# Kernel optimization log

Hardware: AMD Instinct MI355X
Metric: run time of the kernel (lower is better)

## Reference

```python
import jax, jax.numpy as jnp
import numpy as np

N, F, E, B, D = 100000, 256, 128, 10000, 32
GAMMA, ZETA = -0.1, 1.1  # hard-concrete stretch params of L0Dense


def setup_inputs() -> dict:
    key = jax.random.key(0)
    ks = jax.random.split(key, 12)
    return {
        "nodes": jax.random.randint(ks[0], (B,), 0, N),
        "neigh_idx": jax.random.randint(ks[1], (B, D), 0, N),
        "neigh_mask": jax.random.bernoulli(ks[2], 0.9, (B, D)),
        "feature": jax.random.normal(ks[3], (N, F), jnp.float32),
        "W": jax.random.normal(ks[4], (F, E), jnp.float32) * 0.05,
        "b": jnp.zeros((E,), jnp.float32),
        "qz_loga": jax.random.normal(ks[5], (F,), jnp.float32),
        "att1_w": jax.random.normal(ks[6], (2 * E, E), jnp.float32) * 0.05,
        "att1_b": jnp.zeros((E,), jnp.float32),
        "att2_w": jax.random.normal(ks[7], (E, E), jnp.float32) * 0.05,
        "att2_b": jnp.zeros((E,), jnp.float32),
        "att3_w": jax.random.normal(ks[8], (E, 1), jnp.float32) * 0.05,
        "att3_b": jnp.zeros((1,), jnp.float32),
    }


def reference(nodes, neigh_idx, neigh_mask, feature, W, b, qz_loga,
              att1_w, att1_b, att2_w, att2_b, att3_w, att3_b):
    # L0Dense, deterministic (eval) hard-concrete gate on input dims
    z = jnp.clip(jax.nn.sigmoid(qz_loga) * (ZETA - GAMMA) + GAMMA, 0.0, 1.0)
    We = W * z[:, None]                                  # [F, E]

    node_feat = feature[nodes] @ We + b                   # [B, E]
    neigh_feat = feature[neigh_idx] @ We + b              # [B, D, E]

    # GraphRec-style attention MLP over (neighbor, center) pairs
    h = jnp.concatenate(
        [neigh_feat, jnp.broadcast_to(node_feat[:, None, :], neigh_feat.shape)],
        axis=-1)                                          # [B, D, 2E]
    h = jax.nn.relu(h @ att1_w + att1_b)
    h = jax.nn.relu(h @ att2_w + att2_b)
    scores = (h @ att3_w + att3_b)[..., 0]                # [B, D]
    scores = jnp.where(neigh_mask, scores, -1e30)
    att = jax.nn.softmax(scores, axis=-1)                 # [B, D]

    agg = jnp.einsum('bd,bde->be', att, neigh_feat)       # weighted sum
    has_neigh = neigh_mask.any(axis=-1, keepdims=True)
    return jnp.where(has_neigh, agg, node_feat)           # n==0 fallback
```

## Files before the change

### kernel.cpp

```cpp
#include <hip/hip_runtime.h>
#include <hip/hip_bf16.h>
#include <math.h>

#define NN 100000
#define FF 256
#define EE 128
#define BB_ 10000
#define DD 32

typedef __attribute__((ext_vector_type(8))) short short8;
typedef __attribute__((ext_vector_type(4))) float f32x4;

__device__ __forceinline__ short f2bf(float f) {
  union { float f; unsigned u; } v; v.f = f;
  unsigned r = v.u + 0x7fffu + ((v.u >> 16) & 1u);
  return (short)(r >> 16);
}
__device__ __forceinline__ float bf2f(short s) {
  union { unsigned u; float f; } v;
  v.u = ((unsigned)(unsigned short)s) << 16;
  return v.f;
}

__global__ __launch_bounds__(256) void k_prep(
    const float* __restrict__ W, const float* __restrict__ qz,
    const float* __restrict__ a1w, const float* __restrict__ a2w,
    short* __restrict__ WeT, short* __restrict__ a1wTn,
    short* __restrict__ a1wTc, short* __restrict__ w2T) {
  int i = blockIdx.x * 256 + threadIdx.x;
  if (i < 32768) {
    int e = i >> 8, f = i & 255;
    float g = qz[f];
    float s = 1.0f / (1.0f + expf(-g));
    float z = fminf(fmaxf(s * 1.2f - 0.1f, 0.0f), 1.0f);
    WeT[e * 256 + f] = f2bf(W[f * 128 + e] * z);
  } else if (i < 49152) {
    int t = i - 32768; int n = t >> 7, k = t & 127;
    a1wTn[n * 128 + k] = f2bf(a1w[k * 128 + n]);
  } else if (i < 65536) {
    int t = i - 49152; int n = t >> 7, k = t & 127;
    a1wTc[n * 128 + k] = f2bf(a1w[(128 + k) * 128 + n]);
  } else if (i < 81920) {
    int t = i - 65536; int n = t >> 7, k = t & 127;
    w2T[n * 128 + k] = f2bf(a2w[k * 128 + n]);
  }
}

template <int K, bool AF32, bool OUTBF16>
__global__ __launch_bounds__(256) void k_mm(
    const void* __restrict__ Ap, const short* __restrict__ BT,
    const float* __restrict__ bias, const int* __restrict__ idx,
    void* __restrict__ Cp, int M) {
  __shared__ short As[128 * 64];
  __shared__ short Bs[128 * 64];
  const int tid = threadIdx.x;
  const int mb = blockIdx.x * 128;
  const int wave = tid >> 6, lane = tid & 63;
  const int wr = wave >> 1, wc = wave & 1;
  const int l15 = lane & 15, lg = lane >> 4;

  size_t abase[4];
#pragma unroll
  for (int s = 0; s < 4; ++s) {
    int row = (tid + s * 256) >> 3;
    int grow = mb + row;
    int gr = 0;
    if (grow < M) gr = idx ? idx[grow] : grow;
    abase[s] = (size_t)gr * K;
  }

  f32x4 acc[4][4];
#pragma unroll
  for (int i = 0; i < 4; ++i)
#pragma unroll
    for (int j = 0; j < 4; ++j) acc[i][j] = (f32x4){0.f, 0.f, 0.f, 0.f};

  for (int k0 = 0; k0 < K; k0 += 64) {
#pragma unroll
    for (int s = 0; s < 4; ++s) {
      int q = tid + s * 256;
      int row = q >> 3, c = q & 7;
      short8 av;
      if (AF32) {
        const float* ap = (const float*)Ap + abase[s] + k0 + c * 8;
        float4 f0 = *(const float4*)ap;
        float4 f1 = *(const float4*)(ap + 4);
        av[0] = f2bf(f0.x); av[1] = f2bf(f0.y);
        av[2] = f2bf(f0.z); av[3] = f2bf(f0.w);
        av[4] = f2bf(f1.x); av[5] = f2bf(f1.y);
        av[6] = f2bf(f1.z); av[7] = f2bf(f1.w);
      } else {
        av = *(const short8*)((const short*)Ap + abase[s] + k0 + c * 8);
      }
      *(short8*)(As + row * 64 + 8 * (c ^ (row & 7))) = av;
      short8 bv = *(const short8*)(BT + (size_t)row * K + k0 + c * 8);
      *(short8*)(Bs + row * 64 + 8 * (c ^ (row & 7))) = bv;
    }
    __syncthreads();
#pragma unroll
    for (int ks = 0; ks < 2; ++ks) {
      int c = ks * 4 + lg;
      short8 af[4], bfv[4];
#pragma unroll
      for (int i = 0; i < 4; ++i) {
        int r = wr * 64 + i * 16 + l15;
        af[i] = *(short8*)(As + r * 64 + 8 * (c ^ (r & 7)));
        int n = wc * 64 + i * 16 + l15;
        bfv[i] = *(short8*)(Bs + n * 64 + 8 * (c ^ (n & 7)));
      }
#pragma unroll
      for (int i = 0; i < 4; ++i)
#pragma unroll
        for (int j = 0; j < 4; ++j)
          acc[i][j] = __builtin_amdgcn_mfma_f32_16x16x32_bf16(
              af[i], bfv[j], acc[i][j], 0, 0, 0);
    }
    __syncthreads();
  }

  float bv4[4];
#pragma unroll
  for (int j = 0; j < 4; ++j) {
    int col = wc * 64 + j * 16 + l15;
    bv4[j] = bias ? bias[col] : 0.f;
  }
#pragma unroll
  for (int i = 0; i < 4; ++i) {
#pragma unroll
    for (int r = 0; r < 4; ++r) {
      int row = mb + wr * 64 + i * 16 + lg * 4 + r;
      if (row < M) {
#pragma unroll
        for (int j = 0; j < 4; ++j) {
          int col = wc * 64 + j * 16 + l15;
          float v = acc[i][j][r] + bv4[j];
          if (OUTBF16)
            ((short*)Cp)[(size_t)row * EE + col] = f2bf(v);
          else
            ((float*)Cp)[(size_t)row * EE + col] = v;
        }
      }
    }
  }
}

__global__ __launch_bounds__(256) void k_attn2(
    const short* __restrict__ X, const short* __restrict__ Y,
    const float* __restrict__ P, const int* __restrict__ nodes,
    const int* __restrict__ nidx, const int* __restrict__ nmask,
    const short* __restrict__ w2T, const float* __restrict__ b2,
    const float* __restrict__ w3, const float* __restrict__ b3,
    float* __restrict__ out) {
  __shared__ short h1s[128 * 128];
  __shared__ int nidx_s[128];
  __shared__ float scores_s[256];
  __shared__ float atts_s[128];
  __shared__ int has_sh[4];
  const int tid = threadIdx.x;
  const int b0 = blockIdx.x * 4;
  const int wave = tid >> 6, lane = tid & 63;
  const int wr = wave >> 1, wc = wave & 1;
  const int l15 = lane & 15, lg = lane >> 4;

  if (tid < 128) nidx_s[tid] = nidx[b0 * DD + tid];
  __syncthreads();

#pragma unroll
  for (int s = 0; s < 8; ++s) {
    int q = tid + s * 256;
    int row = q >> 4, c = q & 15;
    int n = nidx_s[row];
    short8 yv = *(const short8*)(Y + (size_t)n * EE + c * 8);
    const float* pp = P + (size_t)(b0 + (row >> 5)) * EE + c * 8;
    float4 p0 = *(const float4*)pp;
    float4 p1 = *(const float4*)(pp + 4);
    float pf[8] = {p0.x, p0.y, p0.z, p0.w, p1.x, p1.y, p1.z, p1.w};
    short8 hv;
#pragma unroll
    for (int j = 0; j < 8; ++j)
      hv[j] = f2bf(fmaxf(bf2f(yv[j]) + pf[j], 0.f));
    *(short8*)(h1s + row * 128 + 8 * ((c & 8) | ((c ^ row) & 7))) = hv;
  }
  __syncthreads();

  f32x4 acc[4][4];
#pragma unroll
  for (int i = 0; i < 4; ++i)
#pragma unroll
    for (int j = 0; j < 4; ++j) acc[i][j] = (f32x4){0.f, 0.f, 0.f, 0.f};

#pragma unroll
  for (int ks = 0; ks < 4; ++ks) {
    int c = ks * 4 + lg;
    short8 af[4], bfv[4];
#pragma unroll
    for (int i = 0; i < 4; ++i) {
      int r = wr * 64 + i * 16 + l15;
      af[i] = *(short8*)(h1s + r * 128 + 8 * ((c & 8) | ((c ^ r) & 7)));
      int n = wc * 64 + i * 16 + l15;
      bfv[i] = *(const short8*)(w2T + n * 128 + c * 8);
    }
#pragma unroll
    for (int i = 0; i < 4; ++i)
#pragma unroll
      for (int j = 0; j < 4; ++j)
        acc[i][j] = __builtin_amdgcn_mfma_f32_16x16x32_bf16(
            af[i], bfv[j], acc[i][j], 0, 0, 0);
  }

  float b2v[4], w3v[4];
#pragma unroll
  for (int j = 0; j < 4; ++j) {
    int col = wc * 64 + j * 16 + l15;
    b2v[j] = b2[col];
    w3v[j] = w3[col];
  }
  float part[16];
#pragma unroll
  for (int i = 0; i < 4; ++i)
#pragma unroll
    for (int r = 0; r < 4; ++r) {
      float s = 0.f;
#pragma unroll
      for (int j = 0; j < 4; ++j)
        s += fmaxf(acc[i][j][r] + b2v[j], 0.f) * w3v[j];
      part[i * 4 + r] = s;
    }
#pragma unroll
  for (int off = 1; off <= 8; off <<= 1) {
#pragma unroll
    for (int t = 0; t < 16; ++t) part[t] += __shfl_xor(part[t], off);
  }
  if (l15 == 0) {
#pragma unroll
    for (int i = 0; i < 4; ++i)
#pragma unroll
      for (int r = 0; r < 4; ++r) {
        int row = wr * 64 + i * 16 + lg * 4 + r;
        scores_s[row * 2 + wc] = part[i * 4 + r];
      }
  }
  __syncthreads();

  float b3v = b3[0];
  if (lane < 32) {
    int row = wave * 32 + lane;
    int m = nmask[(size_t)(b0 + wave) * DD + lane];
    float s = scores_s[row * 2] + scores_s[row * 2 + 1] + b3v;
    if (!m) s = -1e30f;
    float mx = s;
#pragma unroll
    for (int off = 1; off <= 16; off <<= 1) mx = fmaxf(mx, __shfl_xor(mx, off));
    float e = expf(s - mx);
    float sum = e;
#pragma unroll
    for (int off = 1; off <= 16; off <<= 1) sum += __shfl_xor(sum, off);
    atts_s[row] = e / sum;
    unsigned long long bal = __ballot(m != 0);
    if (lane == 0) has_sh[wave] = (bal != 0ull) ? 1 : 0;
  }
  __syncthreads();

  {
    int g = wave;
    float a0 = 0.f, a1 = 0.f;
    if (has_sh[g]) {
#pragma unroll 4
      for (int d = 0; d < 32; ++d) {
        float a = atts_s[g * 32 + d];
        const short* xr = X + (size_t)nidx_s[g * 32 + d] * EE;
        a0 += a * bf2f(xr[lane]);
        a1 += a * bf2f(xr[lane + 64]);
      }
    } else {
      const short* xr = X + (size_t)nodes[b0 + g] * EE;
      a0 = bf2f(xr[lane]);
      a1 = bf2f(xr[lane + 64]);
    }
    out[(size_t)(b0 + g) * EE + lane] = a0;
    out[(size_t)(b0 + g) * EE + lane + 64] = a1;
  }
}

extern "C" void kernel_launch(void* const* d_in, const int* in_sizes, int n_in,
                              void* d_out, int out_size, void* d_ws,
                              size_t ws_size, hipStream_t stream) {
  const int* nodes = (const int*)d_in[0];
  const int* nidx = (const int*)d_in[1];
  const int* nmask = (const int*)d_in[2];
  const float* feature = (const float*)d_in[3];
  const float* W = (const float*)d_in[4];
  const float* bb = (const float*)d_in[5];
  const float* qz = (const float*)d_in[6];
  const float* a1w = (const float*)d_in[7];
  const float* a1b = (const float*)d_in[8];
  const float* a2w = (const float*)d_in[9];
  const float* a2b = (const float*)d_in[10];
  const float* a3w = (const float*)d_in[11];
  const float* a3b = (const float*)d_in[12];
  float* out = (float*)d_out;

  char* ws = (char*)d_ws;
  short* WeT   = (short*)(ws);
  short* a1wTn = (short*)(ws + 65536);
  short* a1wTc = (short*)(ws + 98304);
  short* w2T   = (short*)(ws + 131072);
  short* Xb    = (short*)(ws + 163840);
  short* Yb    = (short*)(ws + 163840 + 25600000);
  float* Pv    = (float*)(ws + 163840 + 51200000);

  k_prep<<<320, 256, 0, stream>>>(W, qz, a1w, a2w, WeT, a1wTn, a1wTc, w2T);
  k_mm<256, true, true><<<(NN + 127) / 128, 256, 0, stream>>>(
      feature, WeT, bb, nullptr, Xb, NN);
  k_mm<128, false, true><<<(NN + 127) / 128, 256, 0, stream>>>(
      Xb, a1wTn, a1b, nullptr, Yb, NN);
  k_mm<128, false, false><<<(BB_ + 127) / 128, 256, 0, stream>>>(
      Xb, a1wTc, nullptr, nodes, Pv, BB_);
  k_attn2<<<BB_ / 4, 256, 0, stream>>>(Xb, Yb, Pv, nodes, nidx, nmask, w2T,
                                       a2b, a3w, a3b, out);
}
```

Baseline: 123.8 us.

## Restructure attention kernel to one batch row per wave without LDS staging

The attention kernel now gives each wave one center node with its 32 neighbours. The first-layer activations are built directly in registers as MFMA A operands, instead of being staged through a 32KB swizzled LDS tile. This removes most shared memory use and all block-wide barriers. In exchange, each wave loads the full w2T B operand on its own. It relies on wave-synchronous LDS ordering for its small index and score arrays. The float-to-bf16 helper now uses the HIP intrinsic, and the gather and output stores are widened to 32-bit and float2 accesses.

Result: slower. 130.4 us (+5.3%).

```diff
diff --git a/kernel.cpp b/kernel.cpp
--- a/kernel.cpp
+++ b/kernel.cpp
@@ -12,9 +12,9 @@
 typedef __attribute__((ext_vector_type(4))) float f32x4;
 
 __device__ __forceinline__ short f2bf(float f) {
-  union { float f; unsigned u; } v; v.f = f;
-  unsigned r = v.u + 0x7fffu + ((v.u >> 16) & 1u);
-  return (short)(r >> 16);
+  __hip_bfloat16 h = __float2bfloat16(f);
+  union { __hip_bfloat16 h; short s; } u; u.h = h;
+  return u.s;
 }
 __device__ __forceinline__ float bf2f(short s) {
   union { unsigned u; float f; } v;
@@ -144,142 +144,128 @@
   }
 }
 
-__global__ __launch_bounds__(256) void k_attn2(
+__global__ __launch_bounds__(256) void k_attn3(
     const short* __restrict__ X, const short* __restrict__ Y,
     const float* __restrict__ P, const int* __restrict__ nodes,
     const int* __restrict__ nidx, const int* __restrict__ nmask,
     const short* __restrict__ w2T, const float* __restrict__ b2,
     const float* __restrict__ w3, const float* __restrict__ b3,
     float* __restrict__ out) {
-  __shared__ short h1s[128 * 128];
-  __shared__ int nidx_s[128];
-  __shared__ float scores_s[256];
-  __shared__ float atts_s[128];
-  __shared__ int has_sh[4];
+  __shared__ int ni_s[4][32];
+  __shared__ float sc_s[4][32];
+  __shared__ float att_s[4][32];
   const int tid = threadIdx.x;
-  const int b0 = blockIdx.x * 4;
   const int wave = tid >> 6, lane = tid & 63;
-  const int wr = wave >> 1, wc = wave & 1;
+  const int b = blockIdx.x * 4 + wave;
   const int l15 = lane & 15, lg = lane >> 4;
 
-  if (tid < 128) nidx_s[tid] = nidx[b0 * DD + tid];
-  __syncthreads();
-
-#pragma unroll
-  for (int s = 0; s < 8; ++s) {
-    int q = tid + s * 256;
-    int row = q >> 4, c = q & 15;
-    int n = nidx_s[row];
-    short8 yv = *(const short8*)(Y + (size_t)n * EE + c * 8);
-    const float* pp = P + (size_t)(b0 + (row >> 5)) * EE + c * 8;
-    float4 p0 = *(const float4*)pp;
-    float4 p1 = *(const float4*)(pp + 4);
-    float pf[8] = {p0.x, p0.y, p0.z, p0.w, p1.x, p1.y, p1.z, p1.w};
-    short8 hv;
+  if (lane < 32) ni_s[wave][lane] = nidx[b * DD + lane];
+
+  const int nid0 = ni_s[wave][l15];
+  const int nid1 = ni_s[wave][16 + l15];
+  const short* yr0 = Y + (size_t)nid0 * EE;
+  const short* yr1 = Y + (size_t)nid1 * EE;
+  const float* pr = P + (size_t)b * EE;
+
+  f32x4 acc[2][8];
+#pragma unroll
+  for (int i = 0; i < 2; ++i)
+#pragma unroll
+    for (int j = 0; j < 8; ++j) acc[i][j] = (f32x4){0.f, 0.f, 0.f, 0.f};
+
+#pragma unroll
+  for (int ks = 0; ks < 4; ++ks) {
+    const int k0 = ks * 32 + lg * 8;
+    short8 y0 = *(const short8*)(yr0 + k0);
+    short8 y1 = *(const short8*)(yr1 + k0);
+    float4 pa = *(const float4*)(pr + k0);
+    float4 pb = *(const float4*)(pr + k0 + 4);
+    float pf[8] = {pa.x, pa.y, pa.z, pa.w, pb.x, pb.y, pb.z, pb.w};
+    short8 a0, a1;
+#pragma unroll
+    for (int e = 0; e < 8; ++e) {
+      a0[e] = f2bf(fmaxf(bf2f(y0[e]) + pf[e], 0.f));
+      a1[e] = f2bf(fmaxf(bf2f(y1[e]) + pf[e], 0.f));
+    }
+    short8 bfv[8];
 #pragma unroll
     for (int j = 0; j < 8; ++j)
-      hv[j] = f2bf(fmaxf(bf2f(yv[j]) + pf[j], 0.f));
-    *(short8*)(h1s + row * 128 + 8 * ((c & 8) | ((c ^ row) & 7))) = hv;
-  }
-  __syncthreads();
-
-  f32x4 acc[4][4];
-#pragma unroll
-  for (int i = 0; i < 4; ++i)
-#pragma unroll
-    for (int j = 0; j < 4; ++j) acc[i][j] = (f32x4){0.f, 0.f, 0.f, 0.f};
-
-#pragma unroll
-  for (int ks = 0; ks < 4; ++ks) {
-    int c = ks * 4 + lg;
-    short8 af[4], bfv[4];
-#pragma unroll
-    for (int i = 0; i < 4; ++i) {
-      int r = wr * 64 + i * 16 + l15;
-      af[i] = *(short8*)(h1s + r * 128 + 8 * ((c & 8) | ((c ^ r) & 7)));
-      int n = wc * 64 + i * 16 + l15;
-      bfv[i] = *(const short8*)(w2T + n * 128 + c * 8);
-    }
-#pragma unroll
-    for (int i = 0; i < 4; ++i)
-#pragma unroll
-      for (int j = 0; j < 4; ++j)
-        acc[i][j] = __builtin_amdgcn_mfma_f32_16x16x32_bf16(
-            af[i], bfv[j], acc[i][j], 0, 0, 0);
-  }
-
-  float b2v[4], w3v[4];
-#pragma unroll
-  for (int j = 0; j < 4; ++j) {
-    int col = wc * 64 + j * 16 + l15;
+      bfv[j] = *(const short8*)(w2T + (size_t)(j * 16 + l15) * EE + k0);
+    __builtin_amdgcn_s_setprio(1);
+#pragma unroll
+    for (int j = 0; j < 8; ++j) {
+      acc[0][j] = __builtin_amdgcn_mfma_f32_16x16x32_bf16(a0, bfv[j],
+                                                          acc[0][j], 0, 0, 0);
+      acc[1][j] = __builtin_amdgcn_mfma_f32_16x16x32_bf16(a1, bfv[j],
+                                                          acc[1][j], 0, 0, 0);
+    }
+    __builtin_amdgcn_s_setprio(0);
+  }
+
+  float b2v[8], w3v[8];
+#pragma unroll
+  for (int j = 0; j < 8; ++j) {
+    int col = j * 16 + l15;
     b2v[j] = b2[col];
     w3v[j] = w3[col];
   }
-  float part[16];
-#pragma unroll
-  for (int i = 0; i < 4; ++i)
+  float part[2][4];
+#pragma unroll
+  for (int i = 0; i < 2; ++i)
 #pragma unroll
     for (int r = 0; r < 4; ++r) {
       float s = 0.f;
 #pragma unroll
-      for (int j = 0; j < 4; ++j)
+      for (int j = 0; j < 8; ++j)
         s += fmaxf(acc[i][j][r] + b2v[j], 0.f) * w3v[j];
-      part[i * 4 + r] = s;
+      part[i][r] = s;
     }
 #pragma unroll
   for (int off = 1; off <= 8; off <<= 1) {
 #pragma unroll
-    for (int t = 0; t < 16; ++t) part[t] += __shfl_xor(part[t], off);
+    for (int i = 0; i < 2; ++i)
+#pragma unroll
+      for (int r = 0; r < 4; ++r) part[i][r] += __shfl_xor(part[i][r], off);
   }
   if (l15 == 0) {
 #pragma unroll
-    for (int i = 0; i < 4; ++i)
-#pragma unroll
-      for (int r = 0; r < 4; ++r) {
-        int row = wr * 64 + i * 16 + lg * 4 + r;
-        scores_s[row * 2 + wc] = part[i * 4 + r];
-      }
-  }
-  __syncthreads();
-
-  float b3v = b3[0];
-  if (lane < 32) {
-    int row = wave * 32 + lane;
-    int m = nmask[(size_t)(b0 + wave) * DD + lane];
-    float s = scores_s[row * 2] + scores_s[row * 2 + 1] + b3v;
-    if (!m) s = -1e30f;
-    float mx = s;
-#pragma unroll
-    for (int off = 1; off <= 16; off <<= 1) mx = fmaxf(mx, __shfl_xor(mx, off));
-    float e = expf(s - mx);
-    float sum = e;
-#pragma unroll
-    for (int off = 1; off <= 16; off <<= 1) sum += __shfl_xor(sum, off);
-    atts_s[row] = e / sum;
-    unsigned long long bal = __ballot(m != 0);
-    if (lane == 0) has_sh[wave] = (bal != 0ull) ? 1 : 0;
-  }
-  __syncthreads();
-
-  {
-    int g = wave;
-    float a0 = 0.f, a1 = 0.f;
-    if (has_sh[g]) {
+    for (int i = 0; i < 2; ++i)
+#pragma unroll
+      for (int r = 0; r < 4; ++r)
+        sc_s[wave][i * 16 + lg * 4 + r] = part[i][r];
+  }
+
+  const int row = lane & 31;
+  const int m = nmask[(size_t)b * DD + row];
+  float s = sc_s[wave][row] + b3[0];
+  if (!m) s = -1e30f;
+  float mx = s;
+#pragma unroll
+  for (int off = 1; off <= 16; off <<= 1) mx = fmaxf(mx, __shfl_xor(mx, off));
+  float e = expf(s - mx);
+  float sum = e;
+#pragma unroll
+  for (int off = 1; off <= 16; off <<= 1) sum += __shfl_xor(sum, off);
+  if (lane < 32) att_s[wave][row] = e / sum;
+  const bool has = (__ballot(m != 0) != 0ull);
+
+  float a0 = 0.f, a1 = 0.f;
+  if (has) {
 #pragma unroll 4
-      for (int d = 0; d < 32; ++d) {
-        float a = atts_s[g * 32 + d];
-        const short* xr = X + (size_t)nidx_s[g * 32 + d] * EE;
-        a0 += a * bf2f(xr[lane]);
-        a1 += a * bf2f(xr[lane + 64]);
-      }
-    } else {
-      const short* xr = X + (size_t)nodes[b0 + g] * EE;
-      a0 = bf2f(xr[lane]);
-      a1 = bf2f(xr[lane + 64]);
-    }
-    out[(size_t)(b0 + g) * EE + lane] = a0;
-    out[(size_t)(b0 + g) * EE + lane + 64] = a1;
-  }
+    for (int d = 0; d < 32; ++d) {
+      float a = att_s[wave][d];
+      const short* xr = X + (size_t)ni_s[wave][d] * EE;
+      unsigned xv = *(const unsigned*)(xr + 2 * lane);
+      a0 += a * bf2f((short)(xv & 0xffffu));
+      a1 += a * bf2f((short)(xv >> 16));
+    }
+  } else {
+    const short* xr = X + (size_t)nodes[b] * EE;
+    unsigned xv = *(const unsigned*)(xr + 2 * lane);
+    a0 = bf2f((short)(xv & 0xffffu));
+    a1 = bf2f((short)(xv >> 16));
+  }
+  *(float2*)(out + (size_t)b * EE + 2 * lane) = make_float2(a0, a1);
 }
 
 extern "C" void kernel_launch(void* const* d_in, const int* in_sizes, int n_in,
@@ -316,6 +302,6 @@
       Xb, a1wTn, a1b, nullptr, Yb, NN);
   k_mm<128, false, false><<<(BB_ + 127) / 128, 256, 0, stream>>>(
       Xb, a1wTc, nullptr, nodes, Pv, BB_);
-  k_attn2<<<BB_ / 4, 256, 0, stream>>>(Xb, Yb, Pv, nodes, nidx, nmask, w2T,
+  k_attn3<<<BB_ / 4, 256, 0, stream>>>(Xb, Yb, Pv, nodes, nidx, nmask, w2T,
                                        a2b, a3w, a3b, out);
 }
```
